# Optimization experiments

Hardware: AMD Instinct MI355X
Metric: run time of the kernel (lower is better)

## Reference

```python
import jax, jax.numpy as jnp
import numpy as np

D = 768


def _rope(x):
    # interleaved RoPE over the FULL hidden dim (applied before head split, as in source)
    S, d = x.shape[-2], x.shape[-1]
    pos = jnp.arange(S, dtype=x.dtype)[:, None]                      # [S,1]
    theta = jnp.power(jnp.asarray(10000.0, x.dtype),
                      -2.0 * jnp.arange(d // 2, dtype=x.dtype) / d)  # [d/2]
    ang = pos * theta                                                # [S,d/2]
    cos2 = jnp.repeat(jnp.cos(ang), 2, axis=-1)                      # [S,d]
    sin2 = jnp.repeat(jnp.sin(ang), 2, axis=-1)
    x2 = jnp.stack([-x[..., 1::2], x[..., ::2]], axis=-1).reshape(x.shape)
    return x * cos2 + x2 * sin2


def _attn(q_in, kv_in, wq, bq, wk, bk, wv, bv, n_heads):
    # shared core of SelfAttention (n_heads=1) and MultiheadAttention (n_heads=8)
    B, Sq, Dm = q_in.shape
    Sk = kv_in.shape[1]
    Q = _rope(q_in @ wq + bq)
    K = _rope(kv_in @ wk + bk)
    V = kv_in @ wv + bv
    hd = Dm // n_heads
    Q = Q.reshape(B, Sq, n_heads, hd).transpose(0, 2, 1, 3)
    K = K.reshape(B, Sk, n_heads, hd).transpose(0, 2, 1, 3)
    V = V.reshape(B, Sk, n_heads, hd).transpose(0, 2, 1, 3)
    scores = jnp.einsum('bhqd,bhkd->bhqk', Q, K) * 8.0  # source multiplies by 8, no 1/sqrt(d)
    p = jax.nn.softmax(scores, axis=-1)
    out = jnp.einsum('bhqk,bhkd->bhqd', p, V)
    return out.transpose(0, 2, 1, 3).reshape(B, Sq, Dm)


def _ffn(x, w1, b1, w2, b2):
    return jax.nn.silu(x @ w1 + b1) @ w2 + b2


def _gate(x):
    # F = F * softmax(F, -1) + F
    return x * jax.nn.softmax(x, axis=-1) + x


def setup_inputs() -> dict:
    key = jax.random.key(0)
    ks = jax.random.split(key, 32)
    B, S, L = 32, 512, 100
    s = 1.0 / np.sqrt(D)

    def lin(k):
        kw, kb = jax.random.split(k)
        return (jax.random.normal(kw, (D, D), jnp.float32) * s,
                jax.random.normal(kb, (D,), jnp.float32) * 0.01)

    inp = {}
    inp['text_embedding'] = jax.random.normal(ks[0], (B, S, D), jnp.float32)
    inp['visual_ids'] = jax.random.randint(ks[1], (B, S), 0, L)
    inp['acoustic_ids'] = jax.random.randint(ks[2], (B, S), 0, L)
    # embedding tables (label_size+1 rows, last row is padding_idx -> zeros)
    vt = jax.random.normal(ks[3], (L + 1, D), jnp.float32)
    at = jax.random.normal(ks[4], (L + 1, D), jnp.float32)
    inp['vis_table'] = vt.at[L].set(0.0)
    inp['ac_table'] = at.at[L].set(0.0)
    (inp['hv_wq'], inp['hv_bq']) = lin(ks[5])
    (inp['hv_wk'], inp['hv_bk']) = lin(ks[6])
    (inp['hv_wv'], inp['hv_bv']) = lin(ks[7])
    (inp['ha_wq'], inp['ha_bq']) = lin(ks[8])
    (inp['ha_wk'], inp['ha_bk']) = lin(ks[9])
    (inp['ha_wv'], inp['ha_bv']) = lin(ks[10])
    (inp['ht_wq'], inp['ht_bq']) = lin(ks[11])
    (inp['ht_wk'], inp['ht_bk']) = lin(ks[12])
    (inp['ht_wv'], inp['ht_bv']) = lin(ks[13])
    (inp['ht_fcw'], inp['ht_fcb']) = lin(ks[14])
    (inp['ffn_w1'], inp['ffn_b1']) = lin(ks[15])
    (inp['ffn_w2'], inp['ffn_b2']) = lin(ks[16])
    kw, kb = jax.random.split(ks[17])
    inp['cat_w'] = jax.random.normal(kw, (2 * D, D), jnp.float32) * (1.0 / np.sqrt(2 * D))
    inp['cat_b'] = jax.random.normal(kb, (D,), jnp.float32) * 0.01
    return inp


def reference(text_embedding, vis_table, ac_table,
              hv_wq, hv_bq, hv_wk, hv_bk, hv_wv, hv_bv,
              ha_wq, ha_bq, ha_wk, ha_bk, ha_wv, ha_bv,
              ht_wq, ht_bq, ht_wk, ht_bk, ht_wv, ht_bv, ht_fcw, ht_fcb,
              ffn_w1, ffn_b1, ffn_w2, ffn_b2, cat_w, cat_b,
              visual_ids, acoustic_ids):
    hv = lambda q, kv: _attn(q, kv, hv_wq, hv_bq, hv_wk, hv_bk, hv_wv, hv_bv, 1)
    ha = lambda q, kv: _attn(q, kv, ha_wq, ha_bq, ha_wk, ha_bk, ha_wv, ha_bv, 1)

    visual_ = vis_table[visual_ids]       # [B,S,D]
    acoustic_ = ac_table[acoustic_ids]

    visual_ = hv(text_embedding, visual_)
    acoustic_ = ha(text_embedding, acoustic_)

    F1 = jnp.concatenate([visual_, acoustic_], axis=-1) @ cat_w + cat_b
    F1 = _ffn(_gate(F1), ffn_w1, ffn_b1, ffn_w2, ffn_b2)

    v = hv(visual_, acoustic_)
    a = ha(acoustic_, visual_)
    F2 = jnp.concatenate([v, a], axis=-1) @ cat_w + cat_b
    F2 = _ffn(_gate(F2), ffn_w1, ffn_b1, ffn_w2, ffn_b2)

    F3 = _attn(F1, text_embedding, ht_wq, ht_bq, ht_wk, ht_bk, ht_wv, ht_bv, 8)
    F3 = F3 @ ht_fcw + ht_fcb
    F3 = _ffn(_gate(F3), ffn_w1, ffn_b1, ffn_w2, ffn_b2)

    es = text_embedding + F1 + F2 + F3
    return _gate(es)
```

## Files before the change

kernel.cpp:

```cpp
#include <hip/hip_runtime.h>
#include <stdint.h>
#include <math.h>


typedef unsigned short USH;
typedef __attribute__((ext_vector_type(8))) short short8;
typedef __attribute__((ext_vector_type(4))) float floatx4;

#define MFMA16(a, b, c) __builtin_amdgcn_mfma_f32_16x16x32_bf16((a), (b), (c), 0, 0, 0)

static constexpr int NB = 32;
static constexpr int SS = 512;
static constexpr int DD = 768;
static constexpr int MM = NB * SS;

__device__ __forceinline__ float bf2f(USH h) {
    return __uint_as_float(((unsigned)h) << 16);
}
__device__ __forceinline__ USH f2bf(float x) {
    unsigned u = __float_as_uint(x);
    return (USH)((u + 0x7fffu + ((u >> 16) & 1u)) >> 16);
}
__device__ __forceinline__ void split3(float x, USH &h, USH &m, USH &l) {
    h = f2bf(x);
    const float r1 = x - bf2f(h);
    m = f2bf(r1);
    const float r2 = r1 - bf2f(m);
    l = f2bf(r2);
}
__device__ __forceinline__ void split3x8(const float* v, short8 &H, short8 &M, short8 &L) {
#pragma unroll
    for (int j = 0; j < 8; ++j) {
        USH h, m, l;
        split3(v[j], h, m, l);
        H[j] = (short)h; M[j] = (short)m; L[j] = (short)l;
    }
}
__device__ __forceinline__ uint2 pk4(USH a, USH b, USH c, USH d) {
    uint2 r;
    r.x = (unsigned)a | ((unsigned)b << 16);
    r.y = (unsigned)c | ((unsigned)d << 16);
    return r;
}

struct TransArgs {
    const float* in[13];
    USH* o0[13]; USH* o1[13]; USH* o2[13];
    int R[13];
};

__global__ __launch_bounds__(256) void trans_k(TransArgs a) {
    const int mi = blockIdx.z;
    const float* __restrict__ in = a.in[mi];
    USH* __restrict__ o0 = a.o0[mi];
    USH* __restrict__ o1 = a.o1[mi];
    USH* __restrict__ o2 = a.o2[mi];
    const int R = a.R[mi];
    const int bx = blockIdx.x, by = blockIdx.y;
    if (bx * 32 >= R) return;
    __shared__ float t[32][33];
    const int tx = threadIdx.x & 31, ty = threadIdx.x >> 5;
#pragma unroll
    for (int i = 0; i < 4; ++i)
        t[ty + i * 8][tx] = in[(size_t)(bx * 32 + ty + i * 8) * 768 + by * 32 + tx];
    __syncthreads();
#pragma unroll
    for (int i = 0; i < 4; ++i) {
        USH h, m, l;
        split3(t[tx][ty + i * 8], h, m, l);
        const size_t o = (size_t)(by * 32 + ty + i * 8) * R + bx * 32 + tx;
        o0[o] = h; o1[o] = m; o2[o] = l;
    }
}

__global__ __launch_bounds__(256) void gather_k(const int* __restrict__ ids,
                                                const float* __restrict__ table,
                                                float* __restrict__ dst) {
    const int g  = blockIdx.x * 256 + threadIdx.x;
    const int m  = g / 192;
    const int c4 = (g - m * 192) * 4;
    const int id = ids[m];
    *(float4*)(dst + (size_t)m * DD + c4) =
        *(const float4*)(table + (size_t)id * DD + c4);
}

__global__ __launch_bounds__(256) void tab_k(float* __restrict__ tab) {
    const int p = blockIdx.x * 256 + threadIdx.x;
    const int s = p / 384;
    const int i = p - s * 384;
    const float ef = (-2.0f * (float)i) / 768.0f;
    const float th = (float)pow(10000.0, (double)ef);
    const float ang = (float)s * th;
    float sn, cs;
    sincosf(ang, &sn, &cs);
    tab[2 * p]     = cs;
    tab[2 * p + 1] = sn;
}

__global__ __launch_bounds__(256) void rope_k(float* __restrict__ X) {
    const int p = blockIdx.x * 256 + threadIdx.x;
    const int m = p / 384;
    const int i = p - m * 384;
    const int s = m & (SS - 1);
    const float ef = (-2.0f * (float)i) / 768.0f;
    const float th = (float)pow(10000.0, (double)ef);
    const float ang = (float)s * th;
    float sn, cs;
    sincosf(ang, &sn, &cs);
    float2 x = *(float2*)(X + (size_t)m * DD + 2 * i);
    float2 y;
    y.x = x.x * cs - x.y * sn;
    y.y = x.y * cs + x.x * sn;
    *(float2*)(X + (size_t)m * DD + 2 * i) = y;
}

__global__ __launch_bounds__(256) void gemm_k(
    const float* __restrict__ A0, const float* __restrict__ A1,
    const USH* __restrict__ B0, const USH* __restrict__ B1, const USH* __restrict__ B2,
    int ldb, const float* __restrict__ bias,
    float* __restrict__ C, USH* __restrict__ S0p, USH* __restrict__ S1p,
    USH* __restrict__ S2p, const float* __restrict__ tab,
    int K, int act, int tout, int rope, int Mc)
{
    __shared__ __align__(16) USH smem[24576];
    USH* const sA0 = smem;
    USH* const sA1 = smem + 4096;
    USH* const sA2 = smem + 8192;
    USH* const sB0 = smem + 12288;
    USH* const sB1 = smem + 16384;
    USH* const sB2 = smem + 20480;

    const int tid  = threadIdx.x;
    const int lane = tid & 63;
    const int w    = tid >> 6;
    const int quad = lane >> 4, l15 = lane & 15;
    const int wm = (w >> 1) * 64, wn = (w & 1) * 64;

    const int nbx = gridDim.x;
    const int tot = nbx * (int)gridDim.y;
    int bid = blockIdx.y * nbx + blockIdx.x;
    if ((tot & 7) == 0) bid = (bid & 7) * (tot >> 3) + (bid >> 3);
    const int byy = bid / nbx;
    const int gm0 = (bid - byy * nbx) * 128, gn0 = byy * 128;

    const int i0 = tid * 2, i1 = tid * 2 + 1;
    const int r0 = i0 >> 2, c0 = (i0 & 3) << 3;
    const int r1 = i1 >> 2, c1 = (i1 & 3) << 3;

    const floatx4 zero = {0.f, 0.f, 0.f, 0.f};
    floatx4 acc[4][4];
#pragma unroll
    for (int i = 0; i < 4; ++i)
#pragma unroll
        for (int j = 0; j < 4; ++j) acc[i][j] = zero;

    for (int k0 = 0; k0 < K; k0 += 32) {
        const float* __restrict__ A = (k0 < 768) ? A0 : A1;
        const int kof = (k0 < 768) ? k0 : (k0 - 768);

        *(uint4*)&sB0[r0 * 32 + c0] = *(const uint4*)(B0 + (size_t)(gn0 + r0) * ldb + k0 + c0);
        *(uint4*)&sB0[r1 * 32 + c1] = *(const uint4*)(B0 + (size_t)(gn0 + r1) * ldb + k0 + c1);
        *(uint4*)&sB1[r0 * 32 + c0] = *(const uint4*)(B1 + (size_t)(gn0 + r0) * ldb + k0 + c0);
        *(uint4*)&sB1[r1 * 32 + c1] = *(const uint4*)(B1 + (size_t)(gn0 + r1) * ldb + k0 + c1);
        *(uint4*)&sB2[r0 * 32 + c0] = *(const uint4*)(B2 + (size_t)(gn0 + r0) * ldb + k0 + c0);
        *(uint4*)&sB2[r1 * 32 + c1] = *(const uint4*)(B2 + (size_t)(gn0 + r1) * ldb + k0 + c1);

#pragma unroll
        for (int u = 0; u < 4; ++u) {
            const int idx = tid + u * 256;
            const int r = idx >> 3, c = (idx & 7) * 4;
            const float4 v = *(const float4*)(A + (size_t)(gm0 + r) * 768 + kof + c);
            USH h[4], m[4], l[4];
            split3(v.x, h[0], m[0], l[0]);
            split3(v.y, h[1], m[1], l[1]);
            split3(v.z, h[2], m[2], l[2]);
            split3(v.w, h[3], m[3], l[3]);
            *(uint2*)&sA0[r * 32 + c] = pk4(h[0], h[1], h[2], h[3]);
            *(uint2*)&sA1[r * 32 + c] = pk4(m[0], m[1], m[2], m[3]);
            *(uint2*)&sA2[r * 32 + c] = pk4(l[0], l[1], l[2], l[3]);
        }
        __syncthreads();

        short8 a0[4], a1f[4], a2[4], b0[4], b1f[4], b2[4];
#pragma unroll
        for (int t = 0; t < 4; ++t) {
            const int ao = (wm + t * 16 + l15) * 32 + quad * 8;
            const int bo = (wn + t * 16 + l15) * 32 + quad * 8;
            a0[t]  = *(const short8*)&sA0[ao];
            a1f[t] = *(const short8*)&sA1[ao];
            a2[t]  = *(const short8*)&sA2[ao];
            b0[t]  = *(const short8*)&sB0[bo];
            b1f[t] = *(const short8*)&sB1[bo];
            b2[t]  = *(const short8*)&sB2[bo];
        }
#pragma unroll
        for (int i = 0; i < 4; ++i)
#pragma unroll
            for (int j = 0; j < 4; ++j) acc[i][j] = MFMA16(a0[i],  b0[j],  acc[i][j]);
#pragma unroll
        for (int i = 0; i < 4; ++i)
#pragma unroll
            for (int j = 0; j < 4; ++j) acc[i][j] = MFMA16(a0[i],  b1f[j], acc[i][j]);
#pragma unroll
        for (int i = 0; i < 4; ++i)
#pragma unroll
            for (int j = 0; j < 4; ++j) acc[i][j] = MFMA16(a1f[i], b0[j],  acc[i][j]);
#pragma unroll
        for (int i = 0; i < 4; ++i)
#pragma unroll
            for (int j = 0; j < 4; ++j) acc[i][j] = MFMA16(a0[i],  b2[j],  acc[i][j]);
#pragma unroll
        for (int i = 0; i < 4; ++i)
#pragma unroll
            for (int j = 0; j < 4; ++j) acc[i][j] = MFMA16(a2[i],  b0[j],  acc[i][j]);
#pragma unroll
        for (int i = 0; i < 4; ++i)
#pragma unroll
            for (int j = 0; j < 4; ++j) acc[i][j] = MFMA16(a1f[i], b1f[j], acc[i][j]);
        __syncthreads();
    }

    if (tout == 1) {
        USH* const sT = smem;
#pragma unroll
        for (int p = 0; p < 3; ++p) {
            __syncthreads();
#pragma unroll
            for (int j = 0; j < 4; ++j) {
                const int col = gn0 + wn + j * 16 + l15;
                const int cl  = wn + j * 16 + l15;
                const float bv = bias ? bias[col] : 0.0f;
#pragma unroll
                for (int i = 0; i < 4; ++i) {
#pragma unroll
                    for (int r = 0; r < 4; ++r) {
                        const int rl = wm + i * 16 + quad * 4 + r;
                        USH h, m, l;
                        split3(acc[i][j][r] + bv, h, m, l);
                        sT[cl * 144 + rl] = (p == 0) ? h : ((p == 1) ? m : l);
                    }
                }
            }
            __syncthreads();
            USH* const dst = (p == 0) ? S0p : ((p == 1) ? S1p : S2p);
#pragma unroll
            for (int u = 0; u < 8; ++u) {
                const int cc = u * 256 + tid;
                const int cl = cc >> 4, off = (cc & 15) * 8;
                *(short8*)(dst + (size_t)(gn0 + cl) * Mc + gm0 + off) =
                    *(const short8*)&sT[cl * 144 + off];
            }
        }
        return;
    }

#pragma unroll
    for (int j = 0; j < 4; ++j) {
        const int col = gn0 + wn + j * 16 + l15;
        const float bv = bias ? bias[col] : 0.0f;
#pragma unroll
        for (int i = 0; i < 4; ++i) {
#pragma unroll
            for (int r = 0; r < 4; ++r) {
                const int row = gm0 + wm + i * 16 + quad * 4 + r;
                float x = acc[i][j][r] + bv;
                if (act == 1) {
                    const float s = 1.0f / (1.0f + expf(-x));
                    x = x * s;
                }
                if (rope) {
                    const float px = __shfl_xor(x, 1, 64);
                    const float2 t = *(const float2*)(tab +
                        2 * ((row & (SS - 1)) * 384 + (col >> 1)));
                    x = (col & 1) ? (x * t.x + px * t.y)
                                  : (x * t.x - px * t.y);
                }
                if (tout == 3) {
                    USH h, m, l;
                    split3(x, h, m, l);
                    const size_t o = (size_t)row * 768 + col;
                    S0p[o] = h; S1p[o] = m; S2p[o] = l;
                } else if (tout == 2) {
                    C[(size_t)col * Mc + row] = x;
                } else {
                    C[(size_t)row * 768 + col] = x;
                }
            }
        }
    }
}

__global__ __launch_bounds__(256) void attn_fast_k(
    const float* __restrict__ Q,
    const USH* __restrict__ KH, const USH* __restrict__ KM, const USH* __restrict__ KL,
    const USH* __restrict__ VH, const USH* __restrict__ VM, const USH* __restrict__ VL,
    float* __restrict__ O, int H, int hd, int Mc)
{
    __shared__ __align__(16) float S[16][520];
    __shared__ __align__(16) USH P2buf[16 * 520];
    __shared__ float red[16][16];
    __shared__ float stat[16];

    const int tid  = threadIdx.x;
    const int lane = tid & 63;
    const int w    = tid >> 6;
    const int quad = lane >> 4, l15 = lane & 15;

    const int nbx = gridDim.x;
    const int tot = nbx * (int)gridDim.y;
    int bid = blockIdx.y * nbx + blockIdx.x;
    if ((tot & 7) == 0) bid = (bid & 7) * (tot >> 3) + (bid >> 3);
    const int yy = bid / nbx;
    const int q0 = (bid - yy * nbx) * 16;
    const int b = yy / H;
    const int h = yy - b * H;

    const floatx4 zero = {0.f, 0.f, 0.f, 0.f};

    floatx4 acc[8];
#pragma unroll
    for (int t = 0; t < 8; ++t) acc[t] = zero;

    const size_t qbase  = ((size_t)(b * SS + q0 + l15)) * DD + h * hd;
    const size_t kstrip = ((size_t)(b * SS + w * 128 + l15)) * DD + h * hd;
    const int nks = hd >> 5;
    for (int ks = 0; ks < nks; ++ks) {
        const int co = ks * 32 + quad * 8;
        float qv[8];
        *(float4*)&qv[0] = *(const float4*)(Q + qbase + co);
        *(float4*)&qv[4] = *(const float4*)(Q + qbase + co + 4);
        short8 qh, qm, ql;
        split3x8(qv, qh, qm, ql);

        size_t ka = kstrip + co;
        short8 khc = *(const short8*)&KH[ka];
        short8 kmc = *(const short8*)&KM[ka];
        short8 klc = *(const short8*)&KL[ka];
#pragma unroll
        for (int t = 0; t < 8; ++t) {
            short8 khn = khc, kmn = kmc, kln = klc;
            if (t < 7) {
                const size_t kb = ka + (size_t)(t + 1) * 16 * DD;
                khn = *(const short8*)&KH[kb];
                kmn = *(const short8*)&KM[kb];
                kln = *(const short8*)&KL[kb];
            }
            acc[t] = MFMA16(qh, khc, acc[t]);
            acc[t] = MFMA16(qh, kmc, acc[t]);
            acc[t] = MFMA16(qm, khc, acc[t]);
            acc[t] = MFMA16(qh, klc, acc[t]);
            acc[t] = MFMA16(ql, khc, acc[t]);
            acc[t] = MFMA16(qm, kmc, acc[t]);
            __builtin_amdgcn_sched_barrier(0);
            khc = khn; kmc = kmn; klc = kln;
        }
    }
#pragma unroll
    for (int t = 0; t < 8; ++t)
#pragma unroll
        for (int r = 0; r < 4; ++r)
            S[quad * 4 + r][w * 128 + t * 16 + l15] = acc[t][r] * 8.0f;
    __syncthreads();

    const int row = tid >> 4, c16 = tid & 15;
    const int cb = c16 * 32;
    float mx = -3.4e38f;
#pragma unroll 8
    for (int c = 0; c < 32; ++c) mx = fmaxf(mx, S[row][cb + c]);
    red[row][c16] = mx;
    __syncthreads();
    if (c16 == 0) {
        float m2 = red[row][0];
#pragma unroll
        for (int j = 1; j < 16; ++j) m2 = fmaxf(m2, red[row][j]);
        stat[row] = m2;
    }
    __syncthreads();
    mx = stat[row];
    float ev[32];
    float sum = 0.f;
#pragma unroll 8
    for (int c = 0; c < 32; ++c) {
        ev[c] = expf(S[row][cb + c] - mx);
        sum += ev[c];
    }
    red[row][c16] = sum;
    __syncthreads();
    if (c16 == 0) {
        float s2 = 0.f;
#pragma unroll
        for (int j = 0; j < 16; ++j) s2 += red[row][j];
        stat[row] = s2;
    }
    __syncthreads();
    const float den = stat[row];
    USH* const P0 = (USH*)&S[0][0];
    USH* const P1 = P0 + 16 * 520;
    USH* const P2 = P2buf;
#pragma unroll 8
    for (int c = 0; c < 32; ++c) {
        const float pr = ev[c] / den;
        USH hh, mm, ll;
        split3(pr, hh, mm, ll);
        P0[row * 520 + cb + c] = hh;
        P1[row * 520 + cb + c] = mm;
        P2[row * 520 + cb + c] = ll;
    }
    __syncthreads();

    const int nnt = hd >> 4;
    for (int nt = w; nt < nnt; nt += 4) {
        floatx4 o = zero;
        const int colg = h * hd + nt * 16 + l15;
        const size_t vb = (size_t)colg * Mc + b * SS;
#pragma unroll 2
        for (int ks = 0; ks < 16; ++ks) {
            const int ko = ks * 32 + quad * 8;
            const short8 ph = *(const short8*)&P0[l15 * 520 + ko];
            const short8 pm = *(const short8*)&P1[l15 * 520 + ko];
            const short8 pl = *(const short8*)&P2[l15 * 520 + ko];
            const short8 vh = *(const short8*)&VH[vb + ko];
            const short8 vm = *(const short8*)&VM[vb + ko];
            const short8 vl = *(const short8*)&VL[vb + ko];
            o = MFMA16(ph, vh, o);
            o = MFMA16(ph, vm, o);
            o = MFMA16(pm, vh, o);
            o = MFMA16(ph, vl, o);
            o = MFMA16(pl, vh, o);
            o = MFMA16(pm, vm, o);
        }
#pragma unroll
        for (int r = 0; r < 4; ++r) {
            const int orow = b * SS + q0 + quad * 4 + r;
            O[(size_t)orow * 768 + colg] = o[r];
        }
    }
}

__global__ __launch_bounds__(256) void attn_k(
    const float* __restrict__ Q, const float* __restrict__ Kp,
    const float* __restrict__ Vt, float* __restrict__ O,
    int H, int hd, int Mc)
{
    __shared__ __align__(16) float S[16][520];
    __shared__ __align__(16) USH P2buf[16 * 520];
    __shared__ float red[16][16];
    __shared__ float stat[16];

    const int tid  = threadIdx.x;
    const int lane = tid & 63;
    const int w    = tid >> 6;
    const int quad = lane >> 4, l15 = lane & 15;
    const int b = blockIdx.y / H;
    const int h = blockIdx.y - b * H;
    const int q0 = blockIdx.x * 16;

    const floatx4 zero = {0.f, 0.f, 0.f, 0.f};

    floatx4 acc[8];
#pragma unroll
    for (int t = 0; t < 8; ++t) acc[t] = zero;

    const size_t qbase = ((size_t)(b * SS + q0 + l15)) * DD + h * hd;
    const int nks = hd >> 5;
    for (int ks = 0; ks < nks; ++ks) {
        const int co = ks * 32 + quad * 8;
        float qv[8];
        *(float4*)&qv[0] = *(const float4*)(Q + qbase + co);
        *(float4*)&qv[4] = *(const float4*)(Q + qbase + co + 4);
        short8 qh, qm, ql;
        split3x8(qv, qh, qm, ql);
#pragma unroll
        for (int t = 0; t < 8; ++t) {
            const size_t kb = ((size_t)(b * SS + w * 128 + t * 16 + l15)) * DD + h * hd + co;
            float kv[8];
            *(float4*)&kv[0] = *(const float4*)(Kp + kb);
            *(float4*)&kv[4] = *(const float4*)(Kp + kb + 4);
            short8 kh, km, kl;
            split3x8(kv, kh, km, kl);
            acc[t] = MFMA16(qh, kh, acc[t]);
            acc[t] = MFMA16(qh, km, acc[t]);
            acc[t] = MFMA16(qm, kh, acc[t]);
            acc[t] = MFMA16(qh, kl, acc[t]);
            acc[t] = MFMA16(ql, kh, acc[t]);
            acc[t] = MFMA16(qm, km, acc[t]);
        }
    }
#pragma unroll
    for (int t = 0; t < 8; ++t)
#pragma unroll
        for (int r = 0; r < 4; ++r)
            S[quad * 4 + r][w * 128 + t * 16 + l15] = acc[t][r] * 8.0f;
    __syncthreads();

    const int row = tid >> 4, c16 = tid & 15;
    const int cb = c16 * 32;
    float mx = -3.4e38f;
#pragma unroll 8
    for (int c = 0; c < 32; ++c) mx = fmaxf(mx, S[row][cb + c]);
    red[row][c16] = mx;
    __syncthreads();
    if (c16 == 0) {
        float m2 = red[row][0];
#pragma unroll
        for (int j = 1; j < 16; ++j) m2 = fmaxf(m2, red[row][j]);
        stat[row] = m2;
    }
    __syncthreads();
    mx = stat[row];
    float ev[32];
    float sum = 0.f;
#pragma unroll 8
    for (int c = 0; c < 32; ++c) {
        ev[c] = expf(S[row][cb + c] - mx);
        sum += ev[c];
    }
    red[row][c16] = sum;
    __syncthreads();
    if (c16 == 0) {
        float s2 = 0.f;
#pragma unroll
        for (int j = 0; j < 16; ++j) s2 += red[row][j];
        stat[row] = s2;
    }
    __syncthreads();
    const float den = stat[row];
    USH* const P0 = (USH*)&S[0][0];
    USH* const P1 = P0 + 16 * 520;
    USH* const P2 = P2buf;
#pragma unroll 8
    for (int c = 0; c < 32; ++c) {
        const float pr = ev[c] / den;
        USH hh, mm, ll;
        split3(pr, hh, mm, ll);
        P0[row * 520 + cb + c] = hh;
        P1[row * 520 + cb + c] = mm;
        P2[row * 520 + cb + c] = ll;
    }
    __syncthreads();

    const int nnt = hd >> 4;
    for (int nt = w; nt < nnt; nt += 4) {
        floatx4 o = zero;
        const int colg = h * hd + nt * 16 + l15;
        const size_t vb = (size_t)colg * Mc + b * SS;
        for (int ks = 0; ks < 16; ++ks) {
            const int ko = ks * 32 + quad * 8;
            const short8 ph = *(const short8*)&P0[l15 * 520 + ko];
            const short8 pm = *(const short8*)&P1[l15 * 520 + ko];
            const short8 pl = *(const short8*)&P2[l15 * 520 + ko];
            float vv[8];
            *(float4*)&vv[0] = *(const float4*)(Vt + vb + ko);
            *(float4*)&vv[4] = *(const float4*)(Vt + vb + ko + 4);
            short8 vh, vm, vl;
            split3x8(vv, vh, vm, vl);
            o = MFMA16(ph, vh, o);
            o = MFMA16(ph, vm, o);
            o = MFMA16(pm, vh, o);
            o = MFMA16(ph, vl, o);
            o = MFMA16(pl, vh, o);
            o = MFMA16(pm, vm, o);
        }
#pragma unroll
        for (int r = 0; r < 4; ++r) {
            const int orow = b * SS + q0 + quad * 4 + r;
            O[(size_t)orow * 768 + colg] = o[r];
        }
    }
}

__global__ __launch_bounds__(256) void gate_k(float* __restrict__ X) {
    __shared__ float red[256];
    const int r = blockIdx.x, tid = threadIdx.x;
    const size_t base = (size_t)r * DD;
    float x[3];
#pragma unroll
    for (int j = 0; j < 3; ++j) x[j] = X[base + tid + j * 256];
    float mx = fmaxf(x[0], fmaxf(x[1], x[2]));
    red[tid] = mx;
    __syncthreads();
    for (int s = 128; s > 0; s >>= 1) {
        if (tid < s) red[tid] = fmaxf(red[tid], red[tid + s]);
        __syncthreads();
    }
    mx = red[0];
    __syncthreads();
    float e[3];
    float sum = 0.f;
#pragma unroll
    for (int j = 0; j < 3; ++j) { e[j] = expf(x[j] - mx); sum += e[j]; }
    red[tid] = sum;
    __syncthreads();
    for (int s = 128; s > 0; s >>= 1) {
        if (tid < s) red[tid] += red[tid + s];
        __syncthreads();
    }
    const float den = red[0];
#pragma unroll
    for (int j = 0; j < 3; ++j)
        X[base + tid + j * 256] = x[j] * (e[j] / den) + x[j];
}

__global__ __launch_bounds__(256) void final_k(
    const float* __restrict__ text,
    const float* __restrict__ F1, const float* __restrict__ F2,
    const float* __restrict__ F3, float* __restrict__ out)
{
    __shared__ float red[256];
    const int r = blockIdx.x, tid = threadIdx.x;
    const size_t base = (size_t)r * DD;
    float x[3];
#pragma unroll
    for (int j = 0; j < 3; ++j) {
        const int c = tid + j * 256;
        x[j] = ((text[base + c] + F1[base + c]) + F2[base + c]) + F3[base + c];
    }
    float mx = fmaxf(x[0], fmaxf(x[1], x[2]));
    red[tid] = mx;
    __syncthreads();
    for (int s = 128; s > 0; s >>= 1) {
        if (tid < s) red[tid] = fmaxf(red[tid], red[tid + s]);
        __syncthreads();
    }
    mx = red[0];
    __syncthreads();
    float e[3];
    float sum = 0.f;
#pragma unroll
    for (int j = 0; j < 3; ++j) { e[j] = expf(x[j] - mx); sum += e[j]; }
    red[tid] = sum;
    __syncthreads();
    for (int s = 128; s > 0; s >>= 1) {
        if (tid < s) red[tid] += red[tid + s];
        __syncthreads();
    }
    const float den = red[0];
#pragma unroll
    for (int j = 0; j < 3; ++j) {
        const int c = tid + j * 256;
        out[base + c] = x[j] * (e[j] / den) + x[j];
    }
}

extern "C" void kernel_launch(void* const* d_in, const int* in_sizes, int n_in,
                              void* d_out, int out_size, void* d_ws, size_t ws_size,
                              hipStream_t stream)
{
    (void)in_sizes; (void)n_in; (void)out_size;

    const float* text    = (const float*)d_in[0];
    const int*   vis_ids = (const int*)d_in[1];
    const int*   ac_ids  = (const int*)d_in[2];
    const float* vis_tab = (const float*)d_in[3];
    const float* ac_tab  = (const float*)d_in[4];
    const float* hv_wq = (const float*)d_in[5],  *hv_bq = (const float*)d_in[6];
    const float* hv_wk = (const float*)d_in[7],  *hv_bk = (const float*)d_in[8];
    const float* hv_wv = (const float*)d_in[9],  *hv_bv = (const float*)d_in[10];
    const float* ha_wq = (const float*)d_in[11], *ha_bq = (const float*)d_in[12];
    const float* ha_wk = (const float*)d_in[13], *ha_bk = (const float*)d_in[14];
    const float* ha_wv = (const float*)d_in[15], *ha_bv = (const float*)d_in[16];
    const float* ht_wq = (const float*)d_in[17], *ht_bq = (const float*)d_in[18];
    const float* ht_wk = (const float*)d_in[19], *ht_bk = (const float*)d_in[20];
    const float* ht_wv = (const float*)d_in[21], *ht_bv = (const float*)d_in[22];
    const float* ht_fcw = (const float*)d_in[23], *ht_fcb = (const float*)d_in[24];
    const float* ffn_w1 = (const float*)d_in[25], *ffn_b1 = (const float*)d_in[26];
    const float* ffn_w2 = (const float*)d_in[27], *ffn_b2 = (const float*)d_in[28];
    const float* cat_w  = (const float*)d_in[29], *cat_b  = (const float*)d_in[30];

    const size_t SQ   = (size_t)768 * 768;
    const size_t WUSH = 3 * (12 * SQ + (size_t)768 * 1536);
    const size_t TABF = (size_t)512 * 384 * 2;
    int Mc = 0, fast = 0;
    for (int cand = MM; cand >= 512; cand >>= 1) {
        const size_t nf = WUSH * sizeof(USH) + TABF * 4 + (size_t)cand * 768 * 28;
        const size_t ns = WUSH * sizeof(USH) + (size_t)cand * 768 * 24;
        if (nf <= ws_size) { Mc = cand; fast = 1; break; }
        if (ns <= ws_size) { Mc = cand; fast = 0; break; }
    }
    if (Mc == 0) return;
    const int nchunk = MM / Mc;
    const int chB    = Mc / SS;

    USH* p = (USH*)d_ws;
    USH *wt0[13], *wt1[13], *wt2[13];
    for (int i = 0; i < 13; ++i) {
        const size_t sz = (i == 12) ? (size_t)768 * 1536 : SQ;
        wt0[i] = p; p += sz;
        wt1[i] = p; p += sz;
        wt2[i] = p; p += sz;
    }

    TransArgs ta;
    const float* tin[13] = {hv_wq, hv_wk, hv_wv, ha_wq, ha_wk, ha_wv,
                            ht_wq, ht_wk, ht_wv, ht_fcw, ffn_w1, ffn_w2, cat_w};
    for (int i = 0; i < 13; ++i) {
        ta.in[i] = tin[i]; ta.o0[i] = wt0[i]; ta.o1[i] = wt1[i]; ta.o2[i] = wt2[i];
        ta.R[i] = (i == 12) ? 1536 : 768;
    }
    trans_k<<<dim3(48, 24, 13), 256, 0, stream>>>(ta);

    const size_t PSZ = (size_t)Mc * 768;
    const dim3 gg(Mc / 128, DD / 128), gb(256);
    const int ropeg = Mc * 384 / 256;
    const float* NULF = nullptr;
    USH* const NUSH = nullptr;

    if (fast) {
        float* tab = (float*)p;
        float* fp  = tab + TABF;
        float *A_ = fp + 0 * PSZ, *B_ = fp + 1 * PSZ;
        float *C_ = fp + 2 * PSZ, *F_ = fp + 3 * PSZ;
        USH* KH = (USH*)(fp + 4 * PSZ);
        USH* KM = KH + PSZ;  USH* KL = KM + PSZ;
        USH* VH = KL + PSZ;  USH* VM = VH + PSZ;  USH* VL = VM + PSZ;

        tab_k<<<(512 * 384) / 256, 256, 0, stream>>>(tab);

#define GE(A0P, A1P, WI, LDB, BIAS, CP, KK, ACT) \
    gemm_k<<<gg, gb, 0, stream>>>(A0P, A1P, wt0[WI], wt1[WI], wt2[WI], LDB, BIAS, \
                                  CP, NUSH, NUSH, NUSH, tab, KK, ACT, 0, 0, Mc)
#define GQ(A0P, WI, BIAS, CP) \
    gemm_k<<<gg, gb, 0, stream>>>(A0P, NULF, wt0[WI], wt1[WI], wt2[WI], 768, BIAS, \
                                  CP, NUSH, NUSH, NUSH, tab, 768, 0, 0, 1, Mc)
#define GK(A0P, WI, BIAS) \
    gemm_k<<<gg, gb, 0, stream>>>(A0P, NULF, wt0[WI], wt1[WI], wt2[WI], 768, BIAS, \
                                  (float*)nullptr, KH, KM, KL, tab, 768, 0, 3, 1, Mc)
#define GV(A0P, WI, BIAS) \
    gemm_k<<<gg, gb, 0, stream>>>(A0P, NULF, wt0[WI], wt1[WI], wt2[WI], 768, BIAS, \
                                  (float*)nullptr, VH, VM, VL, tab, 768, 0, 1, 0, Mc)
#define ATTNF(QP, OP, HH, HD) \
    attn_fast_k<<<dim3(SS / 16, chB * (HH)), 256, 0, stream>>>(QP, KH, KM, KL, \
                                                  VH, VM, VL, OP, HH, HD, Mc)
#define GATE(XP) gate_k<<<Mc, 256, 0, stream>>>(XP)

        for (int c = 0; c < nchunk; ++c) {
            const float* tx = text + (size_t)c * PSZ;
            const int* vi = vis_ids + (size_t)c * Mc;
            const int* ai = ac_ids  + (size_t)c * Mc;
            float* outc = (float*)d_out + (size_t)c * PSZ;

            gather_k<<<Mc * 192 / 256, 256, 0, stream>>>(vi, vis_tab, A_);
            gather_k<<<Mc * 192 / 256, 256, 0, stream>>>(ai, ac_tab, B_);

            GQ(tx, 0, hv_bq, C_);
            GK(A_, 1, hv_bk);  GV(A_, 2, hv_bv);
            ATTNF(C_, F_, 1, 768);

            GQ(tx, 3, ha_bq, C_);
            GK(B_, 4, ha_bk);  GV(B_, 5, ha_bv);
            ATTNF(C_, A_, 1, 768);

            GQ(F_, 0, hv_bq, C_);
            GK(A_, 1, hv_bk);  GV(A_, 2, hv_bv);
            ATTNF(C_, C_, 1, 768);

            GQ(A_, 3, ha_bq, B_);
            GK(F_, 4, ha_bk);  GV(F_, 5, ha_bv);
            ATTNF(B_, B_, 1, 768);

            GE(F_, A_, 12, 1536, cat_b, outc, 1536, 0);
            GATE(outc);
            GE(outc, NULF, 10, 768, ffn_b1, F_, 768, 1);
            GE(F_, NULF, 11, 768, ffn_b2, A_, 768, 0);

            GE(C_, B_, 12, 1536, cat_b, outc, 1536, 0);
            GATE(outc);
            GE(outc, NULF, 10, 768, ffn_b1, F_, 768, 1);
            GE(F_, NULF, 11, 768, ffn_b2, C_, 768, 0);

            GQ(A_, 6, ht_bq, B_);
            GK(tx, 7, ht_bk);  GV(tx, 8, ht_bv);
            ATTNF(B_, B_, 8, 96);
            GE(B_, NULF, 9, 768, ht_fcb, F_, 768, 0);
            GATE(F_);
            GE(F_, NULF, 10, 768, ffn_b1, B_, 768, 1);
            GE(B_, NULF, 11, 768, ffn_b2, F_, 768, 0);

            final_k<<<Mc, 256, 0, stream>>>(tx, A_, C_, F_, outc);
        }
#undef GE
#undef GQ
#undef GK
#undef GV
#undef ATTNF
#undef GATE
    } else {
        float* fp = (float*)p;
        float *A_ = fp + 0 * PSZ, *B_ = fp + 1 * PSZ, *C_ = fp + 2 * PSZ;
        float *D_ = fp + 3 * PSZ, *E_ = fp + 4 * PSZ, *F_ = fp + 5 * PSZ;

#define GEMM(A0P, A1P, WI, LDB, BIAS, CP, KK, ACT, TOUT) \
    gemm_k<<<gg, gb, 0, stream>>>(A0P, A1P, wt0[WI], wt1[WI], wt2[WI], LDB, BIAS, \
                                  CP, NUSH, NUSH, NUSH, NULF, KK, ACT, TOUT, 0, Mc)
#define ROPE(XP) rope_k<<<ropeg, 256, 0, stream>>>(XP)
#define ATTN(QP, KP, VP, OP, HH, HD) \
    attn_k<<<dim3(SS / 16, chB * (HH)), 256, 0, stream>>>(QP, KP, VP, OP, HH, HD, Mc)
#define GATE(XP) gate_k<<<Mc, 256, 0, stream>>>(XP)

        for (int c = 0; c < nchunk; ++c) {
            const float* tx = text + (size_t)c * PSZ;
            const int* vi = vis_ids + (size_t)c * Mc;
            const int* ai = ac_ids  + (size_t)c * Mc;
            float* outc = (float*)d_out + (size_t)c * PSZ;

            gather_k<<<Mc * 192 / 256, 256, 0, stream>>>(vi, vis_tab, A_);
            gather_k<<<Mc * 192 / 256, 256, 0, stream>>>(ai, ac_tab, B_);

            GEMM(tx, NULF, 0, 768, hv_bq, C_, 768, 0, 0);
            GEMM(A_, NULF, 1, 768, hv_bk, D_, 768, 0, 0);
            GEMM(A_, NULF, 2, 768, hv_bv, E_, 768, 0, 2);
            ROPE(C_); ROPE(D_);
            ATTN(C_, D_, E_, F_, 1, 768);

            GEMM(tx, NULF, 3, 768, ha_bq, C_, 768, 0, 0);
            GEMM(B_, NULF, 4, 768, ha_bk, D_, 768, 0, 0);
            GEMM(B_, NULF, 5, 768, ha_bv, E_, 768, 0, 2);
            ROPE(C_); ROPE(D_);
            ATTN(C_, D_, E_, A_, 1, 768);

            GEMM(F_, NULF, 0, 768, hv_bq, C_, 768, 0, 0);
            GEMM(A_, NULF, 1, 768, hv_bk, D_, 768, 0, 0);
            GEMM(A_, NULF, 2, 768, hv_bv, E_, 768, 0, 2);
            ROPE(C_); ROPE(D_);
            ATTN(C_, D_, E_, C_, 1, 768);

            GEMM(A_, NULF, 3, 768, ha_bq, B_, 768, 0, 0);
            GEMM(F_, NULF, 4, 768, ha_bk, D_, 768, 0, 0);
            GEMM(F_, NULF, 5, 768, ha_bv, E_, 768, 0, 2);
            ROPE(B_); ROPE(D_);
            ATTN(B_, D_, E_, B_, 1, 768);

            GEMM(F_, A_, 12, 1536, cat_b, D_, 1536, 0, 0);
            GATE(D_);
            GEMM(D_, NULF, 10, 768, ffn_b1, E_, 768, 1, 0);
            GEMM(E_, NULF, 11, 768, ffn_b2, F_, 768, 0, 0);

            GEMM(C_, B_, 12, 1536, cat_b, A_, 1536, 0, 0);
            GATE(A_);
            GEMM(A_, NULF, 10, 768, ffn_b1, C_, 768, 1, 0);
            GEMM(C_, NULF, 11, 768, ffn_b2, B_, 768, 0, 0);

            GEMM(F_, NULF, 6, 768, ht_bq, C_, 768, 0, 0);
            GEMM(tx, NULF, 7, 768, ht_bk, D_, 768, 0, 0);
            GEMM(tx, NULF, 8, 768, ht_bv, E_, 768, 0, 2);
            ROPE(C_); ROPE(D_);
            ATTN(C_, D_, E_, C_, 8, 96);
            GEMM(C_, NULF, 9, 768, ht_fcb, A_, 768, 0, 0);
            GATE(A_);
            GEMM(A_, NULF, 10, 768, ffn_b1, C_, 768, 1, 0);
            GEMM(C_, NULF, 11, 768, ffn_b2, D_, 768, 0, 0);

            final_k<<<Mc, 256, 0, stream>>>(tx, F_, B_, D_, outc);
        }
#undef GEMM
#undef ROPE
#undef ATTN
#undef GATE
    }
}
```

Before: 7.309 ms.

## Replace single-head attention kernel with batched GEMM, softmax kernel, and PV GEMM

The four single-head (hd=768) cross-attentions now run as three steps instead of attn_fast_k. A per-batch QK^T GEMM reuses the tiled MFMA gemm_k, with a batch offset on B and a scale of 8, and writes scores to the output buffer. A row softmax kernel then writes the probabilities as three-way bf16 splits into the K buffers, and a second GEMM multiplies P by V using pre-split A operands. gemm_k gains pre-split A input, lda/ldc, a scale and a per-batch B offset. This trades the fused attention for materialized score and probability tensors and extra memory traffic, in exchange for the better tiled GEMM throughput.

```diff
diff --git a/kernel.cpp b/kernel.cpp
--- a/kernel.cpp
+++ b/kernel.cpp
@@ -116,10 +116,14 @@
 
 __global__ __launch_bounds__(256) void gemm_k(
     const float* __restrict__ A0, const float* __restrict__ A1,
+    const USH* __restrict__ AP0, const USH* __restrict__ AP1,
+    const USH* __restrict__ AP2, int lda,
     const USH* __restrict__ B0, const USH* __restrict__ B1, const USH* __restrict__ B2,
-    int ldb, const float* __restrict__ bias,
-    float* __restrict__ C, USH* __restrict__ S0p, USH* __restrict__ S1p,
-    USH* __restrict__ S2p, const float* __restrict__ tab,
+    int ldb, size_t bofs,
+    const float* __restrict__ bias, float scale,
+    float* __restrict__ C, int ldc,
+    USH* __restrict__ S0p, USH* __restrict__ S1p, USH* __restrict__ S2p,
+    const float* __restrict__ tab,
     int K, int act, int tout, int rope, int Mc)
 {
     __shared__ __align__(16) USH smem[24576];
@@ -143,6 +147,14 @@
     const int byy = bid / nbx;
     const int gm0 = (bid - byy * nbx) * 128, gn0 = byy * 128;
 
+    const USH* __restrict__ Bp0 = B0;
+    const USH* __restrict__ Bp1 = B1;
+    const USH* __restrict__ Bp2 = B2;
+    if (bofs) {
+        const size_t ad = (size_t)(gm0 >> 9) * bofs;
+        Bp0 += ad; Bp1 += ad; Bp2 += ad;
+    }
+
     const int i0 = tid * 2, i1 = tid * 2 + 1;
     const int r0 = i0 >> 2, c0 = (i0 & 3) << 3;
     const int r1 = i1 >> 2, c1 = (i1 & 3) << 3;
@@ -155,29 +167,37 @@
         for (int j = 0; j < 4; ++j) acc[i][j] = zero;
 
     for (int k0 = 0; k0 < K; k0 += 32) {
-        const float* __restrict__ A = (k0 < 768) ? A0 : A1;
-        const int kof = (k0 < 768) ? k0 : (k0 - 768);
-
-        *(uint4*)&sB0[r0 * 32 + c0] = *(const uint4*)(B0 + (size_t)(gn0 + r0) * ldb + k0 + c0);
-        *(uint4*)&sB0[r1 * 32 + c1] = *(const uint4*)(B0 + (size_t)(gn0 + r1) * ldb + k0 + c1);
-        *(uint4*)&sB1[r0 * 32 + c0] = *(const uint4*)(B1 + (size_t)(gn0 + r0) * ldb + k0 + c0);
-        *(uint4*)&sB1[r1 * 32 + c1] = *(const uint4*)(B1 + (size_t)(gn0 + r1) * ldb + k0 + c1);
-        *(uint4*)&sB2[r0 * 32 + c0] = *(const uint4*)(B2 + (size_t)(gn0 + r0) * ldb + k0 + c0);
-        *(uint4*)&sB2[r1 * 32 + c1] = *(const uint4*)(B2 + (size_t)(gn0 + r1) * ldb + k0 + c1);
-
-#pragma unroll
-        for (int u = 0; u < 4; ++u) {
-            const int idx = tid + u * 256;
-            const int r = idx >> 3, c = (idx & 7) * 4;
-            const float4 v = *(const float4*)(A + (size_t)(gm0 + r) * 768 + kof + c);
-            USH h[4], m[4], l[4];
-            split3(v.x, h[0], m[0], l[0]);
-            split3(v.y, h[1], m[1], l[1]);
-            split3(v.z, h[2], m[2], l[2]);
-            split3(v.w, h[3], m[3], l[3]);
-            *(uint2*)&sA0[r * 32 + c] = pk4(h[0], h[1], h[2], h[3]);
-            *(uint2*)&sA1[r * 32 + c] = pk4(m[0], m[1], m[2], m[3]);
-            *(uint2*)&sA2[r * 32 + c] = pk4(l[0], l[1], l[2], l[3]);
+        *(uint4*)&sB0[r0 * 32 + c0] = *(const uint4*)(Bp0 + (size_t)(gn0 + r0) * ldb + k0 + c0);
+        *(uint4*)&sB0[r1 * 32 + c1] = *(const uint4*)(Bp0 + (size_t)(gn0 + r1) * ldb + k0 + c1);
+        *(uint4*)&sB1[r0 * 32 + c0] = *(const uint4*)(Bp1 + (size_t)(gn0 + r0) * ldb + k0 + c0);
+        *(uint4*)&sB1[r1 * 32 + c1] = *(const uint4*)(Bp1 + (size_t)(gn0 + r1) * ldb + k0 + c1);
+        *(uint4*)&sB2[r0 * 32 + c0] = *(const uint4*)(Bp2 + (size_t)(gn0 + r0) * ldb + k0 + c0);
+        *(uint4*)&sB2[r1 * 32 + c1] = *(const uint4*)(Bp2 + (size_t)(gn0 + r1) * ldb + k0 + c1);
+
+        if (AP0) {
+            *(uint4*)&sA0[r0 * 32 + c0] = *(const uint4*)(AP0 + (size_t)(gm0 + r0) * lda + k0 + c0);
+            *(uint4*)&sA0[r1 * 32 + c1] = *(const uint4*)(AP0 + (size_t)(gm0 + r1) * lda + k0 + c1);
+            *(uint4*)&sA1[r0 * 32 + c0] = *(const uint4*)(AP1 + (size_t)(gm0 + r0) * lda + k0 + c0);
+            *(uint4*)&sA1[r1 * 32 + c1] = *(const uint4*)(AP1 + (size_t)(gm0 + r1) * lda + k0 + c1);
+            *(uint4*)&sA2[r0 * 32 + c0] = *(const uint4*)(AP2 + (size_t)(gm0 + r0) * lda + k0 + c0);
+            *(uint4*)&sA2[r1 * 32 + c1] = *(const uint4*)(AP2 + (size_t)(gm0 + r1) * lda + k0 + c1);
+        } else {
+            const float* __restrict__ A = (k0 < 768) ? A0 : A1;
+            const int kof = (k0 < 768) ? k0 : (k0 - 768);
+#pragma unroll
+            for (int u = 0; u < 4; ++u) {
+                const int idx = tid + u * 256;
+                const int r = idx >> 3, c = (idx & 7) * 4;
+                const float4 v = *(const float4*)(A + (size_t)(gm0 + r) * 768 + kof + c);
+                USH h[4], m[4], l[4];
+                split3(v.x, h[0], m[0], l[0]);
+                split3(v.y, h[1], m[1], l[1]);
+                split3(v.z, h[2], m[2], l[2]);
+                split3(v.w, h[3], m[3], l[3]);
+                *(uint2*)&sA0[r * 32 + c] = pk4(h[0], h[1], h[2], h[3]);
+                *(uint2*)&sA1[r * 32 + c] = pk4(m[0], m[1], m[2], m[3]);
+                *(uint2*)&sA2[r * 32 + c] = pk4(l[0], l[1], l[2], l[3]);
+            }
         }
         __syncthreads();
 
@@ -236,7 +256,7 @@
                     for (int r = 0; r < 4; ++r) {
                         const int rl = wm + i * 16 + quad * 4 + r;
                         USH h, m, l;
-                        split3(acc[i][j][r] + bv, h, m, l);
+                        split3(acc[i][j][r] * scale + bv, h, m, l);
                         sT[cl * 144 + rl] = (p == 0) ? h : ((p == 1) ? m : l);
                     }
                 }
@@ -263,7 +283,7 @@
 #pragma unroll
             for (int r = 0; r < 4; ++r) {
                 const int row = gm0 + wm + i * 16 + quad * 4 + r;
-                float x = acc[i][j][r] + bv;
+                float x = acc[i][j][r] * scale + bv;
                 if (act == 1) {
                     const float s = 1.0f / (1.0f + expf(-x));
                     x = x * s;
@@ -283,11 +303,44 @@
                 } else if (tout == 2) {
                     C[(size_t)col * Mc + row] = x;
                 } else {
-                    C[(size_t)row * 768 + col] = x;
+                    C[(size_t)row * ldc + col] = x;
                 }
             }
         }
     }
+}
+
+__global__ __launch_bounds__(256) void smax_k(
+    const float* __restrict__ S,
+    USH* __restrict__ P0, USH* __restrict__ P1, USH* __restrict__ P2)
+{
+    __shared__ float red[256];
+    const int row = blockIdx.x, tid = threadIdx.x;
+    const size_t base = (size_t)row * 512;
+    const float a = S[base + tid];
+    const float b = S[base + 256 + tid];
+    red[tid] = fmaxf(a, b);
+    __syncthreads();
+    for (int s = 128; s > 0; s >>= 1) {
+        if (tid < s) red[tid] = fmaxf(red[tid], red[tid + s]);
+        __syncthreads();
+    }
+    const float mx = red[0];
+    __syncthreads();
+    const float e0 = expf(a - mx);
+    const float e1 = expf(b - mx);
+    red[tid] = e0 + e1;
+    __syncthreads();
+    for (int s = 128; s > 0; s >>= 1) {
+        if (tid < s) red[tid] += red[tid + s];
+        __syncthreads();
+    }
+    const float den = red[0];
+    USH h, m, l;
+    split3(e0 / den, h, m, l);
+    P0[base + tid] = h; P1[base + tid] = m; P2[base + tid] = l;
+    split3(e1 / den, h, m, l);
+    P0[base + 256 + tid] = h; P1[base + 256 + tid] = m; P2[base + 256 + tid] = l;
 }
 
 __global__ __launch_bounds__(256) void attn_fast_k(
@@ -717,17 +770,30 @@
         tab_k<<<(512 * 384) / 256, 256, 0, stream>>>(tab);
 
 #define GE(A0P, A1P, WI, LDB, BIAS, CP, KK, ACT) \
-    gemm_k<<<gg, gb, 0, stream>>>(A0P, A1P, wt0[WI], wt1[WI], wt2[WI], LDB, BIAS, \
-                                  CP, NUSH, NUSH, NUSH, tab, KK, ACT, 0, 0, Mc)
+    gemm_k<<<gg, gb, 0, stream>>>(A0P, A1P, NUSH, NUSH, NUSH, 768, \
+        wt0[WI], wt1[WI], wt2[WI], LDB, (size_t)0, BIAS, 1.0f, CP, 768, \
+        NUSH, NUSH, NUSH, tab, KK, ACT, 0, 0, Mc)
 #define GQ(A0P, WI, BIAS, CP) \
-    gemm_k<<<gg, gb, 0, stream>>>(A0P, NULF, wt0[WI], wt1[WI], wt2[WI], 768, BIAS, \
-                                  CP, NUSH, NUSH, NUSH, tab, 768, 0, 0, 1, Mc)
+    gemm_k<<<gg, gb, 0, stream>>>(A0P, NULF, NUSH, NUSH, NUSH, 768, \
+        wt0[WI], wt1[WI], wt2[WI], 768, (size_t)0, BIAS, 1.0f, CP, 768, \
+        NUSH, NUSH, NUSH, tab, 768, 0, 0, 1, Mc)
 #define GK(A0P, WI, BIAS) \
-    gemm_k<<<gg, gb, 0, stream>>>(A0P, NULF, wt0[WI], wt1[WI], wt2[WI], 768, BIAS, \
-                                  (float*)nullptr, KH, KM, KL, tab, 768, 0, 3, 1, Mc)
+    gemm_k<<<gg, gb, 0, stream>>>(A0P, NULF, NUSH, NUSH, NUSH, 768, \
+        wt0[WI], wt1[WI], wt2[WI], 768, (size_t)0, BIAS, 1.0f, (float*)nullptr, 768, \
+        KH, KM, KL, tab, 768, 0, 3, 1, Mc)
 #define GV(A0P, WI, BIAS) \
-    gemm_k<<<gg, gb, 0, stream>>>(A0P, NULF, wt0[WI], wt1[WI], wt2[WI], 768, BIAS, \
-                                  (float*)nullptr, VH, VM, VL, tab, 768, 0, 1, 0, Mc)
+    gemm_k<<<gg, gb, 0, stream>>>(A0P, NULF, NUSH, NUSH, NUSH, 768, \
+        wt0[WI], wt1[WI], wt2[WI], 768, (size_t)0, BIAS, 1.0f, (float*)nullptr, 768, \
+        VH, VM, VL, tab, 768, 0, 1, 0, Mc)
+#define SGEMM(QP) \
+    gemm_k<<<dim3(Mc / 128, 4), gb, 0, stream>>>(QP, NULF, NUSH, NUSH, NUSH, 768, \
+        KH, KM, KL, 768, (size_t)512 * 768, NULF, 8.0f, outc, 512, \
+        NUSH, NUSH, NUSH, tab, 768, 0, 0, 0, Mc)
+#define SMAX() smax_k<<<Mc, 256, 0, stream>>>(outc, KH, KM, KL)
+#define PVG(OP) \
+    gemm_k<<<dim3(Mc / 128, 6), gb, 0, stream>>>(NULF, NULF, KH, KM, KL, 512, \
+        VH, VM, VL, Mc, (size_t)512, NULF, 1.0f, OP, 768, \
+        NUSH, NUSH, NUSH, tab, 512, 0, 0, 0, Mc)
 #define ATTNF(QP, OP, HH, HD) \
     attn_fast_k<<<dim3(SS / 16, chB * (HH)), 256, 0, stream>>>(QP, KH, KM, KL, \
                                                   VH, VM, VL, OP, HH, HD, Mc)
@@ -744,19 +810,19 @@
 
             GQ(tx, 0, hv_bq, C_);
             GK(A_, 1, hv_bk);  GV(A_, 2, hv_bv);
-            ATTNF(C_, F_, 1, 768);
+            SGEMM(C_); SMAX(); PVG(F_);
 
             GQ(tx, 3, ha_bq, C_);
             GK(B_, 4, ha_bk);  GV(B_, 5, ha_bv);
-            ATTNF(C_, A_, 1, 768);
+            SGEMM(C_); SMAX(); PVG(A_);
 
             GQ(F_, 0, hv_bq, C_);
             GK(A_, 1, hv_bk);  GV(A_, 2, hv_bv);
-            ATTNF(C_, C_, 1, 768);
+            SGEMM(C_); SMAX(); PVG(C_);
 
             GQ(A_, 3, ha_bq, B_);
             GK(F_, 4, ha_bk);  GV(F_, 5, ha_bv);
-            ATTNF(B_, B_, 1, 768);
+            SGEMM(B_); SMAX(); PVG(B_);
 
             GE(F_, A_, 12, 1536, cat_b, outc, 1536, 0);
             GATE(outc);
@@ -782,6 +848,9 @@
 #undef GQ
 #undef GK
 #undef GV
+#undef SGEMM
+#undef SMAX
+#undef PVG
 #undef ATTNF
 #undef GATE
     } else {
@@ -790,8 +859,9 @@
         float *D_ = fp + 3 * PSZ, *E_ = fp + 4 * PSZ, *F_ = fp + 5 * PSZ;
 
 #define GEMM(A0P, A1P, WI, LDB, BIAS, CP, KK, ACT, TOUT) \
-    gemm_k<<<gg, gb, 0, stream>>>(A0P, A1P, wt0[WI], wt1[WI], wt2[WI], LDB, BIAS, \
-                                  CP, NUSH, NUSH, NUSH, NULF, KK, ACT, TOUT, 0, Mc)
+    gemm_k<<<gg, gb, 0, stream>>>(A0P, A1P, NUSH, NUSH, NUSH, 768, \
+        wt0[WI], wt1[WI], wt2[WI], LDB, (size_t)0, BIAS, 1.0f, CP, 768, \
+        NUSH, NUSH, NUSH, NULF, KK, ACT, TOUT, 0, Mc)
 #define ROPE(XP) rope_k<<<ropeg, 256, 0, stream>>>(XP)
 #define ATTN(QP, KP, VP, OP, HH, HD) \
     attn_k<<<dim3(SS / 16, chB * (HH)), 256, 0, stream>>>(QP, KP, VP, OP, HH, HD, Mc)
```

Result: faster. 6.467 ms (-11.5%).
